# Optimization experiments

Measured on AMD Instinct MI355X. Metric: run time of the kernel, lower is better.

The kernel has to match this reference:

```python
import jax, jax.numpy as jnp
import numpy as np

C = 1024
H = 16
K = 2  # num_states
B, N = 4, 4096


def setup_inputs() -> dict:
    key = jax.random.key(0)
    ks_ = jax.random.split(key, 12)
    s = 1.0 / np.sqrt(C)
    inp = {
        "x": jax.random.normal(ks_[0], (B, N, C), dtype=jnp.float32),
        "Wq": jax.random.normal(ks_[1], (C, C), dtype=jnp.float32) * s,
        "bq": jnp.zeros((C,), dtype=jnp.float32),
        "Wk": jax.random.normal(ks_[2], (K, C, C), dtype=jnp.float32) * s,
        "bk": jnp.zeros((K, C), dtype=jnp.float32),
        "Wv": jax.random.normal(ks_[3], (K, C, C), dtype=jnp.float32) * s,
        "bv": jnp.zeros((K, C), dtype=jnp.float32),
        "Wo": jax.random.normal(ks_[4], (C, C), dtype=jnp.float32) * s,
        "bo": jnp.zeros((C,), dtype=jnp.float32),
        "ln_g": jnp.ones((C,), dtype=jnp.float32),
        "ln_b": jnp.zeros((C,), dtype=jnp.float32),
    }
    return inp


def _heads(t):
    # [..., n, (h d)] -> [..., h, n, d]
    shp = t.shape
    d = shp[-1] // H
    t = t.reshape(shp[:-1] + (H, d))
    return jnp.swapaxes(t, -2, -3)


def reference(x, Wq, bq, Wk, bk, Wv, bv, Wo, bo, ln_g, ln_b):
    dtype = x.dtype
    # residual single-layer projections (ResidualMLP with num_layers=-1)
    q = x + jnp.einsum('bnc,cd->bnd', x, Wq) + bq
    ks = x[None] + jnp.einsum('bnc,kcd->kbnd', x, Wk) + bk[:, None, None, :]
    vs = x[None] + jnp.einsum('bnc,kcd->kbnd', x, Wv) + bv[:, None, None, :]
    q = _heads(q)        # [b,h,n,d]
    ks = _heads(ks)      # [k,b,h,n,d]
    vs = _heads(vs)      # [k,b,h,n,d]
    scale = 1.0 / jnp.sqrt(jnp.asarray(N, dtype=jnp.float32))
    ks = ks.astype(jnp.float32) * scale
    vs = vs.astype(jnp.float32) * scale
    # per-state KV outer-products: [k,b,h,d,e]
    states = jnp.einsum('kbhnd,kbhne->kbhde', ks, vs)
    state = jnp.prod(states, axis=0)  # [b,h,d,e]
    out = jnp.einsum('bhnd,bhde->bhne', q.astype(jnp.float32), state)
    out = out.astype(dtype)
    # [b,h,n,d] -> [b,n,(h d)]
    out = jnp.swapaxes(out, 1, 2).reshape(x.shape[0], x.shape[1], C)
    # LayerNorm
    mu = jnp.mean(out, axis=-1, keepdims=True)
    var = jnp.var(out, axis=-1, keepdims=True)
    out = (out - mu) / jnp.sqrt(var + 1e-5) * ln_g + ln_b
    out = jnp.einsum('bnc,cd->bnd', out, Wo) + bo
    return out
```

## Files before the change

### kernel.cpp

```cpp
#include <hip/hip_runtime.h>
#include <hip/hip_bf16.h>

typedef __attribute__((ext_vector_type(8))) short bf16x8;
typedef __attribute__((ext_vector_type(4))) float f32x4;
typedef __attribute__((ext_vector_type(4))) short s16x4;

__device__ __forceinline__ short f2bf(float f) {
  union { float f; unsigned u; } v; v.f = f;
  unsigned r = v.u + 0x7fffu + ((v.u >> 16) & 1u);
  return (short)(r >> 16);
}

__device__ __forceinline__ float bf2f(short s) {
  union { float f; unsigned u; } v; v.u = ((unsigned)(unsigned short)s) << 16;
  return v.f;
}

#define GLD_LDS(g, l) __builtin_amdgcn_global_load_lds( \
    (const __attribute__((address_space(1))) void*)(g), \
    (__attribute__((address_space(3))) void*)(l), 16, 0, 0)

__global__ __launch_bounds__(256)
void convt_k(const float* __restrict__ x, short* __restrict__ xb,
             short* __restrict__ xbT, float* __restrict__ s) {
  __shared__ short tile[64][72];
  __shared__ float red[4][64];
  const int b = blockIdx.z;
  const int n0 = blockIdx.y * 64;
  const int c0 = blockIdx.x * 64;
  const int t = threadIdx.x;
  const int nl = t >> 4;
  const int c4 = (t & 15) << 2;
  const float* xp = x + ((size_t)b * 4096 + n0) * 1024 + c0;
#pragma unroll
  for (int i = 0; i < 4; ++i) {
    const int n = nl + 16 * i;
    const float4 v = *(const float4*)(xp + (size_t)n * 1024 + c4);
    s16x4 o;
    o[0] = f2bf(v.x); o[1] = f2bf(v.y); o[2] = f2bf(v.z); o[3] = f2bf(v.w);
    *(s16x4*)(&xb[((size_t)b * 4096 + n0 + n) * 1024 + c0 + c4]) = o;
    *(s16x4*)(&tile[n][c4]) = o;
  }
  __syncthreads();
  const int cll = t >> 4;
  const int n4 = (t & 15) << 2;
#pragma unroll
  for (int i = 0; i < 4; ++i) {
    const int c = cll + 16 * i;
    s16x4 o;
    o[0] = tile[n4 + 0][c]; o[1] = tile[n4 + 1][c];
    o[2] = tile[n4 + 2][c]; o[3] = tile[n4 + 3][c];
    *(s16x4*)(&xbT[((size_t)b * 1024 + c0 + c) * 4096 + n0 + n4]) = o;
  }
  const int part = t >> 6, col = t & 63;
  float cs = 0.f;
#pragma unroll
  for (int i = 0; i < 16; ++i) cs += bf2f(tile[part * 16 + i][col]);
  red[part][col] = cs;
  __syncthreads();
  if (part == 0)
    atomicAdd(&s[b * 1024 + c0 + col],
              red[0][col] + red[1][col] + red[2][col] + red[3][col]);
}

__global__ void twc_k(const float* __restrict__ Wq, const float* __restrict__ Wk,
                      const float* __restrict__ Wv, const float* __restrict__ Wo,
                      const float* __restrict__ lng, short* __restrict__ dst,
                      short* __restrict__ wqn) {
  __shared__ float tile[32][33];
  const int z = blockIdx.z;
  const float* src = (z == 0) ? Wq
                   : (z == 1) ? Wk
                   : (z == 2) ? (Wk + 1048576)
                   : (z == 3) ? Wv
                   : (z == 4) ? (Wv + 1048576)
                   : Wo;
  short* d = dst + (size_t)z * 1048576;
  const int tx = threadIdx.x, ty = threadIdx.y;
  const int c0 = blockIdx.y * 32, d0 = blockIdx.x * 32;
#pragma unroll
  for (int i = 0; i < 4; ++i) {
    const int cc = c0 + ty + i * 8;
    const float v = src[(size_t)cc * 1024 + d0 + tx];
    tile[ty + i * 8][tx] = v;
    if (z == 0)
      wqn[(size_t)cc * 1024 + d0 + tx] = f2bf(v + (cc == d0 + tx ? 1.0f : 0.0f));
  }
  __syncthreads();
#pragma unroll
  for (int i = 0; i < 4; ++i) {
    const int cc = c0 + tx;
    const int dd = d0 + ty + i * 8;
    float v = tile[tx][ty + i * 8];
    if (z < 5) {
      if (cc == dd) v += 1.0f;
    } else {
      v *= lng[cc];
    }
    d[(size_t)dd * 1024 + cc] = f2bf(v);
  }
}

__global__ __launch_bounds__(256)
void gemv_k(const short* __restrict__ wt, const float* __restrict__ s,
            float* __restrict__ u, float* __restrict__ w) {
  const int z = blockIdx.z, b = blockIdx.y;
  const int lane = threadIdx.x & 63, wid = threadIdx.x >> 6;
  const short* W = wt + ((size_t)(z + 1) << 20);
  const float* sb = s + b * 1024;
  float* outp = (z < 2) ? (u + (z * 4 + b) * 1024) : (w + ((z - 2) * 4 + b) * 1024);
#pragma unroll 1
  for (int it = 0; it < 16; ++it) {
    const int d = blockIdx.x * 64 + wid * 16 + it;
    const short* row = W + (size_t)d * 1024 + lane * 16;
    float acc = 0.f;
#pragma unroll
    for (int j = 0; j < 16; ++j) acc += bf2f(row[j]) * sb[lane * 16 + j];
#pragma unroll
    for (int o = 32; o > 0; o >>= 1) acc += __shfl_down(acc, o);
    if (lane == 0) outp[d] = acc;
  }
}

__global__ __launch_bounds__(256)
void ut_k(const float* __restrict__ Wo, const float* __restrict__ lng,
          const float* __restrict__ lnb, const float* __restrict__ bo,
          float* __restrict__ u, float* __restrict__ t) {
  const int dl = threadIdx.x & 63;
  const int dd = blockIdx.x * 64 + dl;
  const int part = threadIdx.x >> 6;
  float su = 0.f, st = 0.f;
  for (int c = part * 256; c < part * 256 + 256; ++c) {
    const float w = Wo[(size_t)c * 1024 + dd];
    su += lng[c] * w;
    st += lnb[c] * w;
  }
  __shared__ float rs[4][64], rt[4][64];
  rs[part][dl] = su; rt[part][dl] = st;
  __syncthreads();
  if (part == 0) {
    su = rs[0][dl] + rs[1][dl] + rs[2][dl] + rs[3][dl];
    st = rt[0][dl] + rt[1][dl] + rt[2][dl] + rt[3][dl];
    u[dd] = su;
    t[dd] = st + bo[dd];
  }
}

__global__ __launch_bounds__(512, 2)
void gram_k(const short* __restrict__ xbT, float* __restrict__ Pg) {
  extern __shared__ short lds[];
  const int tid = threadIdx.x;
  const int lane = tid & 63;
  const int wv = tid >> 6;
  const int wm = wv >> 2;
  const int wn = wv & 3;
  const int swz = ((blockIdx.x & 7) << 5) + (blockIdx.x >> 3);
  const int b = swz >> 6;
  const int kz = (swz >> 4) & 3;
  const int tl = swz & 15;
  const int bm0 = (tl >> 2) << 8, bn0 = (tl & 3) << 8;
  const int koff = kz << 10;
  const short* Ap = xbT + ((size_t)b << 22);
  float* po = Pg + ((size_t)((kz << 2) + b) << 20);

  const int lrow = ((lane >> 3) << 1) | ((lane >> 2) & 1);
  const int kc = ((lane & 3) ^ ((lane >> 3) & 3)) << 3;
  const int cl = lane & 15;
  const int khi = lane >> 4;

  f32x4 acc[8][4];
#pragma unroll
  for (int i = 0; i < 8; ++i)
#pragma unroll
    for (int j = 0; j < 4; ++j) acc[i][j] = f32x4{0.f, 0.f, 0.f, 0.f};

  auto stage = [&](int buf, int t) {
    const int k0 = koff + (t << 5) + kc;
    short* ab = lds + (buf << 14);
    short* bb = ab + 8192;
#pragma unroll
    for (int c = 0; c < 2; ++c) {
      const int un = wv * 2 + c;
      GLD_LDS(Ap + (size_t)(bm0 + (un << 4) + lrow) * 4096 + k0, ab + (un << 9));
      GLD_LDS(Ap + (size_t)(bn0 + (un << 4) + lrow) * 4096 + k0, bb + (un << 9));
    }
  };

  auto compute = [&](int buf) {
    const short* ab = lds + (buf << 14);
    const short* bb = ab + 8192;
    bf16x8 af[8], bfr[4];
#pragma unroll
    for (int i = 0; i < 8; ++i) {
      const int R = (wm << 7) + (i << 4) + cl;
      af[i] = *(const bf16x8*)(ab + (R << 5) + ((khi ^ ((R >> 1) & 3)) << 3));
    }
#pragma unroll
    for (int j = 0; j < 4; ++j) {
      const int C = (wn << 6) + (j << 4) + cl;
      bfr[j] = *(const bf16x8*)(bb + (C << 5) + ((khi ^ ((C >> 1) & 3)) << 3));
    }
#pragma unroll
    for (int i = 0; i < 8; ++i)
#pragma unroll
      for (int j = 0; j < 4; ++j)
        acc[i][j] = __builtin_amdgcn_mfma_f32_16x16x32_bf16(af[i], bfr[j], acc[i][j], 0, 0, 0);
  };

  stage(0, 0);
  stage(1, 1);
  asm volatile("s_waitcnt vmcnt(4)" ::: "memory");
  __builtin_amdgcn_s_barrier();
#pragma unroll 1
  for (int t = 0; t < 30; ++t) {
    stage((t + 2) & 3, t + 2);
    compute(t & 3);
    asm volatile("s_waitcnt vmcnt(4)" ::: "memory");
    __builtin_amdgcn_s_barrier();
  }
  compute(2);
  asm volatile("s_waitcnt vmcnt(0)" ::: "memory");
  __builtin_amdgcn_s_barrier();
  compute(3);

#pragma unroll
  for (int i = 0; i < 8; ++i)
#pragma unroll
    for (int j = 0; j < 4; ++j) {
      const int col = bn0 + (wn << 6) + (j << 4) + cl;
      const int rowb = bm0 + (wm << 7) + (i << 4) + (khi << 2);
#pragma unroll
      for (int r = 0; r < 4; ++r)
        po[(size_t)(rowb + r) * 1024 + col] = acc[i][j][r];
    }
}

__global__ __launch_bounds__(512, 2)
void oat_k(const short* __restrict__ xb, const short* __restrict__ Beff,
           const float* __restrict__ rq, short* __restrict__ oat,
           float* __restrict__ musum, float* __restrict__ sqsum) {
  extern __shared__ short lds[];
  const int tid = threadIdx.x;
  const int lane = tid & 63;
  const int wv = tid >> 6;
  const int wm = wv >> 2;
  const int wn = wv & 3;
  const int swz = ((blockIdx.x & 7) << 5) + (blockIdx.x >> 3);
  const int b = swz >> 6;
  const int tl = swz & 63;
  const int bm0 = (tl >> 2) << 8;
  const int bn0 = (tl & 3) << 8;
  const short* Ap = xb + ((size_t)b << 22);
  const short* Bp = Beff + ((size_t)b << 20);

  const int lrow = ((lane >> 3) << 1) | ((lane >> 2) & 1);
  const int kc = ((lane & 3) ^ ((lane >> 3) & 3)) << 3;
  const int cl = lane & 15;
  const int khi = lane >> 4;

  f32x4 acc[8][4];
#pragma unroll
  for (int i = 0; i < 8; ++i)
#pragma unroll
    for (int j = 0; j < 4; ++j) acc[i][j] = f32x4{0.f, 0.f, 0.f, 0.f};

  auto stage = [&](int buf, int t) {
    const int k0 = (t << 5) + kc;
    short* ab = lds + (buf << 14);
    short* bb = ab + 8192;
#pragma unroll
    for (int c = 0; c < 2; ++c) {
      const int un = wv * 2 + c;
      GLD_LDS(Ap + (size_t)(bm0 + (un << 4) + lrow) * 1024 + k0, ab + (un << 9));
      GLD_LDS(Bp + (size_t)(bn0 + (un << 4) + lrow) * 1024 + k0, bb + (un << 9));
    }
  };

  auto compute = [&](int buf) {
    const short* ab = lds + (buf << 14);
    const short* bb = ab + 8192;
    bf16x8 af[8], bfr[4];
#pragma unroll
    for (int i = 0; i < 8; ++i) {
      const int R = (wm << 7) + (i << 4) + cl;
      af[i] = *(const bf16x8*)(ab + (R << 5) + ((khi ^ ((R >> 1) & 3)) << 3));
    }
#pragma unroll
    for (int j = 0; j < 4; ++j) {
      const int C = (wn << 6) + (j << 4) + cl;
      bfr[j] = *(const bf16x8*)(bb + (C << 5) + ((khi ^ ((C >> 1) & 3)) << 3));
    }
#pragma unroll
    for (int i = 0; i < 8; ++i)
#pragma unroll
      for (int j = 0; j < 4; ++j)
        acc[i][j] = __builtin_amdgcn_mfma_f32_16x16x32_bf16(af[i], bfr[j], acc[i][j], 0, 0, 0);
  };

  stage(0, 0);
  stage(1, 1);
  asm volatile("s_waitcnt vmcnt(4)" ::: "memory");
  __builtin_amdgcn_s_barrier();
#pragma unroll 1
  for (int t = 0; t < 30; ++t) {
    stage((t + 2) & 3, t + 2);
    compute(t & 3);
    asm volatile("s_waitcnt vmcnt(4)" ::: "memory");
    __builtin_amdgcn_s_barrier();
  }
  compute(2);
  asm volatile("s_waitcnt vmcnt(0)" ::: "memory");
  __builtin_amdgcn_s_barrier();
  compute(3);

#pragma unroll
  for (int i = 0; i < 8; ++i) {
    const int rowb = bm0 + (wm << 7) + (i << 4) + (khi << 2);
    s16x4 pk[4];
#pragma unroll
    for (int j = 0; j < 4; ++j) {
      const int col = bn0 + (wn << 6) + (j << 4) + cl;
      const float rqc = rq[b * 1024 + col];
#pragma unroll
      for (int r = 0; r < 4; ++r) pk[j][r] = f2bf(acc[i][j][r] + rqc);
#pragma unroll
      for (int r = 0; r < 4; ++r)
        oat[(size_t)(b * 4096 + rowb + r) * 1024 + col] = pk[j][r];
    }
#pragma unroll
    for (int r = 0; r < 4; ++r) {
      float sv = 0.f, sq = 0.f;
#pragma unroll
      for (int j = 0; j < 4; ++j) {
        const float fv = bf2f(pk[j][r]);
        sv += fv; sq += fv * fv;
      }
#pragma unroll
      for (int m = 1; m < 16; m <<= 1) {
        sv += __shfl_xor(sv, m);
        sq += __shfl_xor(sq, m);
      }
      if (cl == 0) {
        atomicAdd(&musum[b * 4096 + rowb + r], sv);
        atomicAdd(&sqsum[b * 4096 + rowb + r], sq);
      }
    }
  }
}

__global__ __launch_bounds__(256)
void greduce_k(const float* __restrict__ Pg, short* __restrict__ G) {
  const int b = blockIdx.x >> 10;
  const int local = ((blockIdx.x & 1023) << 10) + (threadIdx.x << 2);
  float4 a = {0.f, 0.f, 0.f, 0.f};
#pragma unroll
  for (int kz = 0; kz < 4; ++kz) {
    const float4 v = *(const float4*)(Pg + (((size_t)((kz << 2) + b)) << 20) + local);
    a.x += v.x; a.y += v.y; a.z += v.z; a.w += v.w;
  }
  const float sc = 1.0f / 4096.0f;
  s16x4 o;
  o[0] = f2bf(a.x * sc); o[1] = f2bf(a.y * sc);
  o[2] = f2bf(a.z * sc); o[3] = f2bf(a.w * sc);
  *(s16x4*)(G + ((size_t)b << 20) + local) = o;
}

__global__ __launch_bounds__(256, 2)
void gemm128_k(const short* __restrict__ A, const short* __restrict__ Bt,
               short* __restrict__ out) {
  extern __shared__ short lds[];
  const int bid = blockIdx.x;
  const int swz = ((bid & 7) << 4) + (bid >> 3);
  const int bm0 = (swz >> 3) << 7;
  const int bn0 = (swz & 7) << 7;
  const short* Bp = Bt + ((size_t)blockIdx.y << 20);
  short* op = out + ((size_t)blockIdx.y << 21);
  const int tid = threadIdx.x, lane = tid & 63, wid = tid >> 6;
  const int wm = (wid >> 1) << 6, wn = (wid & 1) << 6;
  const int lrow = ((lane >> 3) << 1) | ((lane >> 2) & 1);
  const int kc = ((lane & 3) ^ ((lane >> 3) & 3)) << 3;
  const int cl = lane & 15, khi = lane >> 4;

  f32x4 acc[4][4];
#pragma unroll
  for (int i = 0; i < 4; ++i)
#pragma unroll
    for (int j = 0; j < 4; ++j) acc[i][j] = f32x4{0.f, 0.f, 0.f, 0.f};

  auto stage = [&](int buf, int t) {
    const int k0 = (t << 5) + kc;
    short* ab = lds + (buf << 13);
    short* bb = ab + 4096;
#pragma unroll
    for (int c = 0; c < 2; ++c) {
      const int un = wid * 2 + c;
      GLD_LDS(A + (size_t)(bm0 + (un << 4) + lrow) * 1024 + k0, ab + (un << 9));
      GLD_LDS(Bp + (size_t)(bn0 + (un << 4) + lrow) * 1024 + k0, bb + (un << 9));
    }
  };

  auto compute = [&](int buf) {
    const short* ab = lds + (buf << 13);
    const short* bb = ab + 4096;
    bf16x8 af[4], bfr[4];
#pragma unroll
    for (int i = 0; i < 4; ++i) {
      const int R = wm + (i << 4) + cl;
      af[i] = *(const bf16x8*)(ab + (R << 5) + ((khi ^ ((R >> 1) & 3)) << 3));
    }
#pragma unroll
    for (int j = 0; j < 4; ++j) {
      const int C = wn + (j << 4) + cl;
      bfr[j] = *(const bf16x8*)(bb + (C << 5) + ((khi ^ ((C >> 1) & 3)) << 3));
    }
#pragma unroll
    for (int i = 0; i < 4; ++i)
#pragma unroll
      for (int j = 0; j < 4; ++j)
        acc[i][j] = __builtin_amdgcn_mfma_f32_16x16x32_bf16(af[i], bfr[j], acc[i][j], 0, 0, 0);
  };

  stage(0, 0);
  stage(1, 1);
  asm volatile("s_waitcnt vmcnt(4)" ::: "memory");
  __builtin_amdgcn_s_barrier();
#pragma unroll 1
  for (int t = 0; t < 30; ++t) {
    stage((t + 2) & 3, t + 2);
    compute(t & 3);
    asm volatile("s_waitcnt vmcnt(4)" ::: "memory");
    __builtin_amdgcn_s_barrier();
  }
  compute(2);
  asm volatile("s_waitcnt vmcnt(0)" ::: "memory");
  __builtin_amdgcn_s_barrier();
  compute(3);

#pragma unroll
  for (int i = 0; i < 4; ++i)
#pragma unroll
    for (int j = 0; j < 4; ++j) {
      const int col = bn0 + wn + (j << 4) + cl;
      const int rowb = bm0 + wm + (i << 4) + (khi << 2);
#pragma unroll
      for (int r = 0; r < 4; ++r)
        op[(size_t)(rowb + r) * 1024 + col] = f2bf(acc[i][j][r]);
    }
}

__global__ __launch_bounds__(256)
void sw_k(const short* __restrict__ wt, const short* __restrict__ Tt,
          const float* __restrict__ u, const float* __restrict__ w,
          const float* __restrict__ bk, const float* __restrict__ bv,
          const short* __restrict__ wqn, const float* __restrict__ bq,
          short* __restrict__ Beff, float* __restrict__ rq) {
  __shared__ short Al[64 * 40];
  __shared__ short Bl[64 * 40];
  __shared__ short S[64][72];
  const int h = blockIdx.x & 15, b = blockIdx.x >> 4;
  const int tid = threadIdx.x, lane = tid & 63, wid = tid >> 6;
  const int srow = tid >> 2, sch = (tid & 3) << 3;
  const int cl = lane & 15, khi = lane >> 4;

  f32x4 acc2[2][4];
#pragma unroll
  for (int k = 0; k < 2; ++k)
#pragma unroll
    for (int j = 0; j < 4; ++j) acc2[k][j] = f32x4{0.f, 0.f, 0.f, 0.f};

#pragma unroll
  for (int k = 0; k < 2; ++k) {
    const short* Ap = wt + ((size_t)(1 + k) << 20) + ((size_t)(h * 64) << 10);
    const short* Bp = Tt + ((size_t)b << 21) + ((size_t)(k * 1024 + h * 64) << 10);
#pragma unroll 1
    for (int ns = 0; ns < 1024; ns += 32) {
      bf16x8 va = *(const bf16x8*)(Ap + ((size_t)srow << 10) + ns + sch);
      bf16x8 vb = *(const bf16x8*)(Bp + ((size_t)srow << 10) + ns + sch);
      __syncthreads();
      *(bf16x8*)(Al + srow * 40 + sch) = va;
      *(bf16x8*)(Bl + srow * 40 + sch) = vb;
      __syncthreads();
      bf16x8 a = *(const bf16x8*)(Al + (wid * 16 + cl) * 40 + (khi << 3));
#pragma unroll
      for (int j = 0; j < 4; ++j) {
        bf16x8 bb = *(const bf16x8*)(Bl + (j * 16 + cl) * 40 + (khi << 3));
        acc2[k][j] = __builtin_amdgcn_mfma_f32_16x16x32_bf16(a, bb, acc2[k][j], 0, 0, 0);
      }
    }
  }

  const int d0 = wid * 16 + (khi << 2);
  const float invN = 1.0f / 4096.0f;
#pragma unroll
  for (int j = 0; j < 4; ++j) {
    const int e = j * 16 + cl;
    s16x4 pk;
#pragma unroll
    for (int r = 0; r < 4; ++r) {
      const int d = d0 + r;
      float m[2];
#pragma unroll
      for (int k = 0; k < 2; ++k) {
        const float bkd = bk[k * 1024 + h * 64 + d];
        const float bve = bv[k * 1024 + h * 64 + e];
        const float ud = u[(k * 4 + b) * 1024 + h * 64 + d];
        const float we = w[(k * 4 + b) * 1024 + h * 64 + e];
        m[k] = acc2[k][j][r] + (ud * bve + bkd * we + 4096.f * bkd * bve) * invN;
      }
      pk[r] = f2bf(m[0] * m[1]);
    }
    *(s16x4*)(&S[e][d0]) = pk;
  }
  __syncthreads();

  if (wid == 0) {
    float acc = 0.f;
#pragma unroll 1
    for (int d = 0; d < 64; ++d) acc += bq[h * 64 + d] * bf2f(S[lane][d]);
    rq[b * 1024 + h * 64 + lane] = acc;
  }
  bf16x8 af[4][2];
#pragma unroll
  for (int mi = 0; mi < 4; ++mi)
#pragma unroll
    for (int kk = 0; kk < 2; ++kk)
      af[mi][kk] = *(const bf16x8*)(&S[mi * 16 + cl][kk * 32 + khi * 8]);
  const short* wq = wqn + h * 64;
  short* bdst = Beff + ((size_t)b << 20) + ((size_t)(h * 64) << 10);
#pragma unroll 1
  for (int nf = 0; nf < 16; ++nf) {
    const int c0 = wid * 256 + nf * 16;
    const bf16x8 bf0 = *(const bf16x8*)(wq + (size_t)(c0 + cl) * 1024 + khi * 8);
    const bf16x8 bf1 = *(const bf16x8*)(wq + (size_t)(c0 + cl) * 1024 + 32 + khi * 8);
    f32x4 a4[4];
#pragma unroll
    for (int mi = 0; mi < 4; ++mi) {
      a4[mi] = f32x4{0.f, 0.f, 0.f, 0.f};
      a4[mi] = __builtin_amdgcn_mfma_f32_16x16x32_bf16(af[mi][0], bf0, a4[mi], 0, 0, 0);
      a4[mi] = __builtin_amdgcn_mfma_f32_16x16x32_bf16(af[mi][1], bf1, a4[mi], 0, 0, 0);
    }
#pragma unroll
    for (int mi = 0; mi < 4; ++mi)
#pragma unroll
      for (int r = 0; r < 4; ++r)
        bdst[(size_t)(mi * 16 + khi * 4 + r) * 1024 + c0 + cl] = f2bf(a4[mi][r]);
  }
}

__global__ __launch_bounds__(512, 2)
void gemmo_k(const short* __restrict__ A, const short* __restrict__ WT,
             const float* __restrict__ musum, const float* __restrict__ sqsum,
             const float* __restrict__ uu, const float* __restrict__ tt,
             float* __restrict__ fout) {
  extern __shared__ short lds[];
  const int tid = threadIdx.x;
  const int lane = tid & 63;
  const int wv = tid >> 6;
  const int wm = wv >> 2;
  const int wn = wv & 3;
  const int swz = ((blockIdx.x & 7) << 5) + (blockIdx.x >> 3);
  const int bm0 = (swz >> 2) << 8;
  const int bn0 = (swz & 3) << 8;

  const int lrow = ((lane >> 3) << 1) | ((lane >> 2) & 1);
  const int kc = ((lane & 3) ^ ((lane >> 3) & 3)) << 3;
  const int cl = lane & 15;
  const int khi = lane >> 4;

  f32x4 acc[8][4];
#pragma unroll
  for (int i = 0; i < 8; ++i)
#pragma unroll
    for (int j = 0; j < 4; ++j) acc[i][j] = f32x4{0.f, 0.f, 0.f, 0.f};

  auto stage = [&](int buf, int t) {
    const int k0 = (t << 5) + kc;
    short* ab = lds + (buf << 14);
    short* bb = ab + 8192;
#pragma unroll
    for (int c = 0; c < 2; ++c) {
      const int un = wv * 2 + c;
      GLD_LDS(A + (size_t)(bm0 + (un << 4) + lrow) * 1024 + k0, ab + (un << 9));
      GLD_LDS(WT + (size_t)(bn0 + (un << 4) + lrow) * 1024 + k0, bb + (un << 9));
    }
  };

  auto compute = [&](int buf) {
    const short* ab = lds + (buf << 14);
    const short* bb = ab + 8192;
    bf16x8 af[8], bfr[4];
#pragma unroll
    for (int i = 0; i < 8; ++i) {
      const int R = (wm << 7) + (i << 4) + cl;
      af[i] = *(const bf16x8*)(ab + (R << 5) + ((khi ^ ((R >> 1) & 3)) << 3));
    }
#pragma unroll
    for (int j = 0; j < 4; ++j) {
      const int C = (wn << 6) + (j << 4) + cl;
      bfr[j] = *(const bf16x8*)(bb + (C << 5) + ((khi ^ ((C >> 1) & 3)) << 3));
    }
#pragma unroll
    for (int i = 0; i < 8; ++i)
#pragma unroll
      for (int j = 0; j < 4; ++j)
        acc[i][j] = __builtin_amdgcn_mfma_f32_16x16x32_bf16(af[i], bfr[j], acc[i][j], 0, 0, 0);
  };

  stage(0, 0);
  stage(1, 1);
  asm volatile("s_waitcnt vmcnt(4)" ::: "memory");
  __builtin_amdgcn_s_barrier();
#pragma unroll 1
  for (int t = 0; t < 30; ++t) {
    stage((t + 2) & 3, t + 2);
    compute(t & 3);
    asm volatile("s_waitcnt vmcnt(4)" ::: "memory");
    __builtin_amdgcn_s_barrier();
  }
  compute(2);
  asm volatile("s_waitcnt vmcnt(0)" ::: "memory");
  __builtin_amdgcn_s_barrier();
  compute(3);

#pragma unroll
  for (int i = 0; i < 8; ++i) {
    const int rowb = bm0 + (wm << 7) + (i << 4) + (khi << 2);
    const float4 ms = *(const float4*)(musum + rowb);
    const float4 qs = *(const float4*)(sqsum + rowb);
    float mu[4], rs[4];
    mu[0] = ms.x * (1.0f / 1024.0f); mu[1] = ms.y * (1.0f / 1024.0f);
    mu[2] = ms.z * (1.0f / 1024.0f); mu[3] = ms.w * (1.0f / 1024.0f);
    rs[0] = rsqrtf(fmaxf(qs.x * (1.0f / 1024.0f) - mu[0] * mu[0], 0.f) + 1e-5f);
    rs[1] = rsqrtf(fmaxf(qs.y * (1.0f / 1024.0f) - mu[1] * mu[1], 0.f) + 1e-5f);
    rs[2] = rsqrtf(fmaxf(qs.z * (1.0f / 1024.0f) - mu[2] * mu[2], 0.f) + 1e-5f);
    rs[3] = rsqrtf(fmaxf(qs.w * (1.0f / 1024.0f) - mu[3] * mu[3], 0.f) + 1e-5f);
#pragma unroll
    for (int j = 0; j < 4; ++j) {
      const int col = bn0 + (wn << 6) + (j << 4) + cl;
      const float uc = uu[col];
      const float tc = tt[col];
#pragma unroll
      for (int r = 0; r < 4; ++r)
        fout[(size_t)(rowb + r) * 1024 + col] = rs[r] * (acc[i][j][r] - mu[r] * uc) + tc;
    }
  }
}

extern "C" void kernel_launch(void* const* d_in, const int* in_sizes, int n_in,
                              void* d_out, int out_size, void* d_ws, size_t ws_size,
                              hipStream_t stream) {
  const float* x = (const float*)d_in[0];
  const float* Wq = (const float*)d_in[1];
  const float* bq = (const float*)d_in[2];
  const float* Wk = (const float*)d_in[3];
  const float* bk = (const float*)d_in[4];
  const float* Wv = (const float*)d_in[5];
  const float* bv = (const float*)d_in[6];
  const float* Wo = (const float*)d_in[7];
  const float* bo = (const float*)d_in[8];
  const float* lng = (const float*)d_in[9];
  const float* lnb = (const float*)d_in[10];

  char* ws = (char*)d_ws;
  short* xb = (short*)(ws + 0);
  short* wt = (short*)(ws + 33554432);
  short* wqn = (short*)(ws + 46137344);
  short* Beff = (short*)(ws + 48234496);
  float* rq = (float*)(ws + 56623104);
  float* musum = (float*)(ws + 56639488);
  float* sqsum = (float*)(ws + 56705024);
  float* s = (float*)(ws + 56770560);
  float* u = (float*)(ws + 56786944);
  float* w = (float*)(ws + 56819712);
  float* uu = (float*)(ws + 56852480);
  float* tt = (float*)(ws + 56856576);
  short* xbT = (short*)(ws + 79691776);
  short* Gt = (short*)(ws + 113246208);
  short* Tt = (short*)(ws + 121634816);
  float* Pg = (float*)(ws + 143351808);
  short* oat = xbT;

  hipMemsetAsync(musum, 0, 147456, stream);
  convt_k<<<dim3(16, 64, 4), 256, 0, stream>>>(x, xb, xbT, s);
  twc_k<<<dim3(32, 32, 6), dim3(32, 8), 0, stream>>>(Wq, Wk, Wv, Wo, lng, wt, wqn);
  gemv_k<<<dim3(16, 4, 4), 256, 0, stream>>>(wt, s, u, w);
  ut_k<<<16, 256, 0, stream>>>(Wo, lng, lnb, bo, uu, tt);

  gram_k<<<256, 512, 131072, stream>>>(xbT, Pg);
  greduce_k<<<4096, 256, 0, stream>>>(Pg, Gt);
  gemm128_k<<<dim3(128, 4), 256, 65536, stream>>>(wt + 3145728, Gt, Tt);
  sw_k<<<64, 256, 0, stream>>>(wt, Tt, u, w, bk, bv, wqn, bq, Beff, rq);

  oat_k<<<256, 512, 131072, stream>>>(xb, Beff, rq, oat, musum, sqsum);
  gemmo_k<<<256, 512, 131072, stream>>>(oat, wt + 5242880, musum, sqsum, uu, tt,
                                        (float*)d_out);
}
```

Before: 271.6 us.

## Compute Q projection explicitly fused with Gram kernel, apply per-head state separately

Instead of folding the state into an effective per-batch weight Beff = (Wq+I)·S and running a full 16384x1024x1024 GEMM per batch, the Q projection is computed once as a batched GEMM, launched in the same grid as the Gram kernel via an interleaved mode bit. A new small attn_k kernel then multiplies each head's Q slice by its 64x64 state with MFMA and accumulates the LayerNorm sums. This drops the Beff construction in sw_k and lets Q overlap with the Gram work. In exchange it adds a q round-trip through memory and one extra kernel launch.

```diff
diff --git a/kernel.cpp b/kernel.cpp
--- a/kernel.cpp
+++ b/kernel.cpp
@@ -65,8 +65,7 @@
 
 __global__ void twc_k(const float* __restrict__ Wq, const float* __restrict__ Wk,
                       const float* __restrict__ Wv, const float* __restrict__ Wo,
-                      const float* __restrict__ lng, short* __restrict__ dst,
-                      short* __restrict__ wqn) {
+                      const float* __restrict__ lng, short* __restrict__ dst) {
   __shared__ float tile[32][33];
   const int z = blockIdx.z;
   const float* src = (z == 0) ? Wq
@@ -79,13 +78,8 @@
   const int tx = threadIdx.x, ty = threadIdx.y;
   const int c0 = blockIdx.y * 32, d0 = blockIdx.x * 32;
 #pragma unroll
-  for (int i = 0; i < 4; ++i) {
-    const int cc = c0 + ty + i * 8;
-    const float v = src[(size_t)cc * 1024 + d0 + tx];
-    tile[ty + i * 8][tx] = v;
-    if (z == 0)
-      wqn[(size_t)cc * 1024 + d0 + tx] = f2bf(v + (cc == d0 + tx ? 1.0f : 0.0f));
-  }
+  for (int i = 0; i < 4; ++i)
+    tile[ty + i * 8][tx] = src[(size_t)(c0 + ty + i * 8) * 1024 + d0 + tx];
   __syncthreads();
 #pragma unroll
   for (int i = 0; i < 4; ++i) {
@@ -147,21 +141,34 @@
 }
 
 __global__ __launch_bounds__(512, 2)
-void gram_k(const short* __restrict__ xbT, float* __restrict__ Pg) {
+void gramq_k(const short* __restrict__ xb, const short* __restrict__ xbT,
+             const short* __restrict__ wtq, const float* __restrict__ bq,
+             short* __restrict__ q, float* __restrict__ Pg) {
   extern __shared__ short lds[];
   const int tid = threadIdx.x;
   const int lane = tid & 63;
   const int wv = tid >> 6;
   const int wm = wv >> 2;
   const int wn = wv & 3;
-  const int swz = ((blockIdx.x & 7) << 5) + (blockIdx.x >> 3);
-  const int b = swz >> 6;
-  const int kz = (swz >> 4) & 3;
-  const int tl = swz & 15;
-  const int bm0 = (tl >> 2) << 8, bn0 = (tl & 3) << 8;
-  const int koff = kz << 10;
-  const short* Ap = xbT + ((size_t)b << 22);
-  float* po = Pg + ((size_t)((kz << 2) + b) << 20);
+  const int mode = blockIdx.x & 1;
+  const int id = blockIdx.x >> 1;
+  const int swz = ((id & 7) << 5) + (id >> 3);
+
+  int bm0, bn0, ld, koff;
+  const short *Ap, *Bp;
+  float* po = nullptr;
+  if (mode == 0) {
+    const int kz = swz & 3, tl = (swz >> 2) & 15, b = swz >> 6;
+    bm0 = (tl >> 2) << 8; bn0 = (tl & 3) << 8;
+    ld = 4096; koff = kz << 10;
+    Ap = xbT + ((size_t)b << 22);
+    Bp = Ap;
+    po = Pg + ((size_t)((kz << 2) + b) << 20);
+  } else {
+    bm0 = (swz & 63) << 8; bn0 = (swz >> 6) << 8;
+    ld = 1024; koff = 0;
+    Ap = xb; Bp = wtq;
+  }
 
   const int lrow = ((lane >> 3) << 1) | ((lane >> 2) & 1);
   const int kc = ((lane & 3) ^ ((lane >> 3) & 3)) << 3;
@@ -181,8 +188,8 @@
 #pragma unroll
     for (int c = 0; c < 2; ++c) {
       const int un = wv * 2 + c;
-      GLD_LDS(Ap + (size_t)(bm0 + (un << 4) + lrow) * 4096 + k0, ab + (un << 9));
-      GLD_LDS(Ap + (size_t)(bn0 + (un << 4) + lrow) * 4096 + k0, bb + (un << 9));
+      GLD_LDS(Ap + (size_t)(bm0 + (un << 4) + lrow) * ld + k0, ab + (un << 9));
+      GLD_LDS(Bp + (size_t)(bn0 + (un << 4) + lrow) * ld + k0, bb + (un << 9));
     }
   };
 
@@ -223,128 +230,29 @@
   __builtin_amdgcn_s_barrier();
   compute(3);
 
-#pragma unroll
-  for (int i = 0; i < 8; ++i)
-#pragma unroll
-    for (int j = 0; j < 4; ++j) {
-      const int col = bn0 + (wn << 6) + (j << 4) + cl;
-      const int rowb = bm0 + (wm << 7) + (i << 4) + (khi << 2);
-#pragma unroll
-      for (int r = 0; r < 4; ++r)
-        po[(size_t)(rowb + r) * 1024 + col] = acc[i][j][r];
-    }
-}
-
-__global__ __launch_bounds__(512, 2)
-void oat_k(const short* __restrict__ xb, const short* __restrict__ Beff,
-           const float* __restrict__ rq, short* __restrict__ oat,
-           float* __restrict__ musum, float* __restrict__ sqsum) {
-  extern __shared__ short lds[];
-  const int tid = threadIdx.x;
-  const int lane = tid & 63;
-  const int wv = tid >> 6;
-  const int wm = wv >> 2;
-  const int wn = wv & 3;
-  const int swz = ((blockIdx.x & 7) << 5) + (blockIdx.x >> 3);
-  const int b = swz >> 6;
-  const int tl = swz & 63;
-  const int bm0 = (tl >> 2) << 8;
-  const int bn0 = (tl & 3) << 8;
-  const short* Ap = xb + ((size_t)b << 22);
-  const short* Bp = Beff + ((size_t)b << 20);
-
-  const int lrow = ((lane >> 3) << 1) | ((lane >> 2) & 1);
-  const int kc = ((lane & 3) ^ ((lane >> 3) & 3)) << 3;
-  const int cl = lane & 15;
-  const int khi = lane >> 4;
-
-  f32x4 acc[8][4];
-#pragma unroll
-  for (int i = 0; i < 8; ++i)
-#pragma unroll
-    for (int j = 0; j < 4; ++j) acc[i][j] = f32x4{0.f, 0.f, 0.f, 0.f};
-
-  auto stage = [&](int buf, int t) {
-    const int k0 = (t << 5) + kc;
-    short* ab = lds + (buf << 14);
-    short* bb = ab + 8192;
-#pragma unroll
-    for (int c = 0; c < 2; ++c) {
-      const int un = wv * 2 + c;
-      GLD_LDS(Ap + (size_t)(bm0 + (un << 4) + lrow) * 1024 + k0, ab + (un << 9));
-      GLD_LDS(Bp + (size_t)(bn0 + (un << 4) + lrow) * 1024 + k0, bb + (un << 9));
-    }
-  };
-
-  auto compute = [&](int buf) {
-    const short* ab = lds + (buf << 14);
-    const short* bb = ab + 8192;
-    bf16x8 af[8], bfr[4];
-#pragma unroll
-    for (int i = 0; i < 8; ++i) {
-      const int R = (wm << 7) + (i << 4) + cl;
-      af[i] = *(const bf16x8*)(ab + (R << 5) + ((khi ^ ((R >> 1) & 3)) << 3));
-    }
-#pragma unroll
-    for (int j = 0; j < 4; ++j) {
-      const int C = (wn << 6) + (j << 4) + cl;
-      bfr[j] = *(const bf16x8*)(bb + (C << 5) + ((khi ^ ((C >> 1) & 3)) << 3));
-    }
+  if (mode == 0) {
 #pragma unroll
     for (int i = 0; i < 8; ++i)
 #pragma unroll
-      for (int j = 0; j < 4; ++j)
-        acc[i][j] = __builtin_amdgcn_mfma_f32_16x16x32_bf16(af[i], bfr[j], acc[i][j], 0, 0, 0);
-  };
-
-  stage(0, 0);
-  stage(1, 1);
-  asm volatile("s_waitcnt vmcnt(4)" ::: "memory");
-  __builtin_amdgcn_s_barrier();
-#pragma unroll 1
-  for (int t = 0; t < 30; ++t) {
-    stage((t + 2) & 3, t + 2);
-    compute(t & 3);
-    asm volatile("s_waitcnt vmcnt(4)" ::: "memory");
-    __builtin_amdgcn_s_barrier();
-  }
-  compute(2);
-  asm volatile("s_waitcnt vmcnt(0)" ::: "memory");
-  __builtin_amdgcn_s_barrier();
-  compute(3);
-
-#pragma unroll
-  for (int i = 0; i < 8; ++i) {
-    const int rowb = bm0 + (wm << 7) + (i << 4) + (khi << 2);
-    s16x4 pk[4];
-#pragma unroll
-    for (int j = 0; j < 4; ++j) {
-      const int col = bn0 + (wn << 6) + (j << 4) + cl;
-      const float rqc = rq[b * 1024 + col];
-#pragma unroll
-      for (int r = 0; r < 4; ++r) pk[j][r] = f2bf(acc[i][j][r] + rqc);
-#pragma unroll
-      for (int r = 0; r < 4; ++r)
-        oat[(size_t)(b * 4096 + rowb + r) * 1024 + col] = pk[j][r];
-    }
-#pragma unroll
-    for (int r = 0; r < 4; ++r) {
-      float sv = 0.f, sq = 0.f;
-#pragma unroll
       for (int j = 0; j < 4; ++j) {
-        const float fv = bf2f(pk[j][r]);
-        sv += fv; sq += fv * fv;
-      }
-#pragma unroll
-      for (int m = 1; m < 16; m <<= 1) {
-        sv += __shfl_xor(sv, m);
-        sq += __shfl_xor(sq, m);
-      }
-      if (cl == 0) {
-        atomicAdd(&musum[b * 4096 + rowb + r], sv);
-        atomicAdd(&sqsum[b * 4096 + rowb + r], sq);
-      }
-    }
+        const int col = bn0 + (wn << 6) + (j << 4) + cl;
+        const int rowb = bm0 + (wm << 7) + (i << 4) + (khi << 2);
+#pragma unroll
+        for (int r = 0; r < 4; ++r)
+          po[(size_t)(rowb + r) * 1024 + col] = acc[i][j][r];
+      }
+  } else {
+#pragma unroll
+    for (int i = 0; i < 8; ++i)
+#pragma unroll
+      for (int j = 0; j < 4; ++j) {
+        const int col = bn0 + (wn << 6) + (j << 4) + cl;
+        const int rowb = bm0 + (wm << 7) + (i << 4) + (khi << 2);
+        const float bi = bq[col];
+#pragma unroll
+        for (int r = 0; r < 4; ++r)
+          q[(size_t)(rowb + r) * 1024 + col] = f2bf(acc[i][j][r] + bi);
+      }
   }
 }
 
@@ -449,14 +357,12 @@
 }
 
 __global__ __launch_bounds__(256)
-void sw_k(const short* __restrict__ wt, const short* __restrict__ Tt,
+void sc_k(const short* __restrict__ wt, const short* __restrict__ Tt,
           const float* __restrict__ u, const float* __restrict__ w,
           const float* __restrict__ bk, const float* __restrict__ bv,
-          const short* __restrict__ wqn, const float* __restrict__ bq,
-          short* __restrict__ Beff, float* __restrict__ rq) {
+          short* __restrict__ stt) {
   __shared__ short Al[64 * 40];
   __shared__ short Bl[64 * 40];
-  __shared__ short S[64][72];
   const int h = blockIdx.x & 15, b = blockIdx.x >> 4;
   const int tid = threadIdx.x, lane = tid & 63, wid = tid >> 6;
   const int srow = tid >> 2, sch = (tid & 3) << 3;
@@ -509,41 +415,86 @@
       }
       pk[r] = f2bf(m[0] * m[1]);
     }
-    *(s16x4*)(&S[e][d0]) = pk;
+    *(s16x4*)(stt + ((size_t)(b * 16 + h) << 12) + (e << 6) + d0) = pk;
+  }
+}
+
+__global__ __launch_bounds__(256)
+void attn_k(const short* __restrict__ q, const short* __restrict__ stt,
+            short* __restrict__ oat, float* __restrict__ musum,
+            float* __restrict__ sqsum) {
+  __shared__ short Al[128 * 72];
+  __shared__ short Bl[64 * 72];
+  const int tid = threadIdx.x;
+  const int lane = tid & 63;
+  const int wid = tid >> 6;
+  const int mc = blockIdx.x;
+  const int bh = blockIdx.y;
+  const int b = bh >> 4, h = bh & 15;
+  const size_t qbase = ((size_t)(b * 4096 + mc * 128)) * 1024 + h * 64;
+#pragma unroll
+  for (int s = 0; s < 4; ++s) {
+    const int idx = tid + s * 256;
+    const int row = idx >> 3, cc = (idx & 7) << 3;
+    *(bf16x8*)(Al + row * 72 + cc) = *(const bf16x8*)(q + qbase + (size_t)row * 1024 + cc);
+  }
+#pragma unroll
+  for (int s = 0; s < 2; ++s) {
+    const int idx = tid + s * 256;
+    const int row = idx >> 3, cc = (idx & 7) << 3;
+    *(bf16x8*)(Bl + row * 72 + cc) = *(const bf16x8*)(stt + (bh << 12) + (row << 6) + cc);
   }
   __syncthreads();
-
-  if (wid == 0) {
-    float acc = 0.f;
-#pragma unroll 1
-    for (int d = 0; d < 64; ++d) acc += bq[h * 64 + d] * bf2f(S[lane][d]);
-    rq[b * 1024 + h * 64 + lane] = acc;
-  }
-  bf16x8 af[4][2];
-#pragma unroll
-  for (int mi = 0; mi < 4; ++mi)
-#pragma unroll
-    for (int kk = 0; kk < 2; ++kk)
-      af[mi][kk] = *(const bf16x8*)(&S[mi * 16 + cl][kk * 32 + khi * 8]);
-  const short* wq = wqn + h * 64;
-  short* bdst = Beff + ((size_t)b << 20) + ((size_t)(h * 64) << 10);
-#pragma unroll 1
-  for (int nf = 0; nf < 16; ++nf) {
-    const int c0 = wid * 256 + nf * 16;
-    const bf16x8 bf0 = *(const bf16x8*)(wq + (size_t)(c0 + cl) * 1024 + khi * 8);
-    const bf16x8 bf1 = *(const bf16x8*)(wq + (size_t)(c0 + cl) * 1024 + 32 + khi * 8);
-    f32x4 a4[4];
-#pragma unroll
-    for (int mi = 0; mi < 4; ++mi) {
-      a4[mi] = f32x4{0.f, 0.f, 0.f, 0.f};
-      a4[mi] = __builtin_amdgcn_mfma_f32_16x16x32_bf16(af[mi][0], bf0, a4[mi], 0, 0, 0);
-      a4[mi] = __builtin_amdgcn_mfma_f32_16x16x32_bf16(af[mi][1], bf1, a4[mi], 0, 0, 0);
-    }
-#pragma unroll
-    for (int mi = 0; mi < 4; ++mi)
-#pragma unroll
-      for (int r = 0; r < 4; ++r)
-        bdst[(size_t)(mi * 16 + khi * 4 + r) * 1024 + c0 + cl] = f2bf(a4[mi][r]);
+  f32x4 acc[2][4];
+#pragma unroll
+  for (int i = 0; i < 2; ++i)
+#pragma unroll
+    for (int j = 0; j < 4; ++j) acc[i][j] = f32x4{0.f, 0.f, 0.f, 0.f};
+#pragma unroll
+  for (int ks = 0; ks < 2; ++ks) {
+    bf16x8 a0 = *(const bf16x8*)(Al + (wid * 32 + (lane & 15)) * 72 + ks * 32 + ((lane >> 4) << 3));
+    bf16x8 a1 = *(const bf16x8*)(Al + (wid * 32 + 16 + (lane & 15)) * 72 + ks * 32 + ((lane >> 4) << 3));
+#pragma unroll
+    for (int j = 0; j < 4; ++j) {
+      bf16x8 bb = *(const bf16x8*)(Bl + (j * 16 + (lane & 15)) * 72 + ks * 32 + ((lane >> 4) << 3));
+      acc[0][j] = __builtin_amdgcn_mfma_f32_16x16x32_bf16(a0, bb, acc[0][j], 0, 0, 0);
+      acc[1][j] = __builtin_amdgcn_mfma_f32_16x16x32_bf16(a1, bb, acc[1][j], 0, 0, 0);
+    }
+  }
+  const int r0 = wid * 32 + ((lane >> 4) << 2);
+  const int cl = lane & 15;
+#pragma unroll
+  for (int i = 0; i < 2; ++i) {
+    s16x4 pk[4];
+#pragma unroll
+    for (int j = 0; j < 4; ++j) {
+#pragma unroll
+      for (int r = 0; r < 4; ++r) pk[j][r] = f2bf(acc[i][j][r]);
+#pragma unroll
+      for (int r = 0; r < 4; ++r) {
+        const int row = b * 4096 + mc * 128 + r0 + i * 16 + r;
+        oat[(size_t)row * 1024 + h * 64 + j * 16 + cl] = pk[j][r];
+      }
+    }
+#pragma unroll
+    for (int r = 0; r < 4; ++r) {
+      float sv = 0.f, sq = 0.f;
+#pragma unroll
+      for (int j = 0; j < 4; ++j) {
+        const float fv = bf2f(pk[j][r]);
+        sv += fv; sq += fv * fv;
+      }
+#pragma unroll
+      for (int m = 1; m < 16; m <<= 1) {
+        sv += __shfl_xor(sv, m);
+        sq += __shfl_xor(sq, m);
+      }
+      if (cl == 0) {
+        const int row = b * 4096 + mc * 128 + r0 + i * 16 + r;
+        atomicAdd(&musum[row], sv);
+        atomicAdd(&sqsum[row], sq);
+      }
+    }
   }
 }
 
@@ -664,34 +615,33 @@
   char* ws = (char*)d_ws;
   short* xb = (short*)(ws + 0);
   short* wt = (short*)(ws + 33554432);
-  short* wqn = (short*)(ws + 46137344);
-  short* Beff = (short*)(ws + 48234496);
-  float* rq = (float*)(ws + 56623104);
-  float* musum = (float*)(ws + 56639488);
-  float* sqsum = (float*)(ws + 56705024);
-  float* s = (float*)(ws + 56770560);
-  float* u = (float*)(ws + 56786944);
-  float* w = (float*)(ws + 56819712);
-  float* uu = (float*)(ws + 56852480);
-  float* tt = (float*)(ws + 56856576);
+  short* q = (short*)(ws + 46137344);
   short* xbT = (short*)(ws + 79691776);
   short* Gt = (short*)(ws + 113246208);
   short* Tt = (short*)(ws + 121634816);
+  short* stt = (short*)(ws + 138412032);
+  float* u = (float*)(ws + 138936320);
+  float* w = (float*)(ws + 138969088);
+  float* uu = (float*)(ws + 139001856);
+  float* tt = (float*)(ws + 139005952);
+  float* s = (float*)(ws + 139010048);
+  float* musum = (float*)(ws + 139026432);
+  float* sqsum = (float*)(ws + 139091968);
   float* Pg = (float*)(ws + 143351808);
   short* oat = xbT;
 
-  hipMemsetAsync(musum, 0, 147456, stream);
+  hipMemsetAsync(s, 0, 147456, stream);
   convt_k<<<dim3(16, 64, 4), 256, 0, stream>>>(x, xb, xbT, s);
-  twc_k<<<dim3(32, 32, 6), dim3(32, 8), 0, stream>>>(Wq, Wk, Wv, Wo, lng, wt, wqn);
+  twc_k<<<dim3(32, 32, 6), dim3(32, 8), 0, stream>>>(Wq, Wk, Wv, Wo, lng, wt);
   gemv_k<<<dim3(16, 4, 4), 256, 0, stream>>>(wt, s, u, w);
   ut_k<<<16, 256, 0, stream>>>(Wo, lng, lnb, bo, uu, tt);
 
-  gram_k<<<256, 512, 131072, stream>>>(xbT, Pg);
+  gramq_k<<<512, 512, 131072, stream>>>(xb, xbT, wt, bq, q, Pg);
   greduce_k<<<4096, 256, 0, stream>>>(Pg, Gt);
   gemm128_k<<<dim3(128, 4), 256, 65536, stream>>>(wt + 3145728, Gt, Tt);
-  sw_k<<<64, 256, 0, stream>>>(wt, Tt, u, w, bk, bv, wqn, bq, Beff, rq);
-
-  oat_k<<<256, 512, 131072, stream>>>(xb, Beff, rq, oat, musum, sqsum);
+  sc_k<<<64, 256, 0, stream>>>(wt, Tt, u, w, bk, bv, stt);
+
+  attn_k<<<dim3(32, 64), 256, 0, stream>>>(q, stt, oat, musum, sqsum);
   gemmo_k<<<256, 512, 131072, stream>>>(oat, wt + 5242880, musum, sqsum, uu, tt,
                                         (float*)d_out);
 }
```

Result: faster. 262.9 us (-3.2%).
